# Performance work log

Hardware: AMD Instinct MI355X
Metric: run time of the kernel (lower is better)

The kernel has to match this reference:

```python
import jax, jax.numpy as jnp
import numpy as np

N = 100000  # number of nodes (batch of Irreps objects)
MUL = {'0e': 128, '1o': 64, '2e': 32}  # multiplicities per irrep id
DIM = {'0e': 1, '1o': 3, '2e': 5}      # 2l+1 per irrep id


def setup_inputs() -> dict:
    key = jax.random.key(0)
    ks = jax.random.split(key, 7)
    x0e = jax.random.normal(ks[0], (N, MUL['0e'], DIM['0e']), dtype=jnp.float32)
    x1o = jax.random.normal(ks[1], (N, MUL['1o'], DIM['1o']), dtype=jnp.float32)
    x2e = jax.random.normal(ks[2], (N, MUL['2e'], DIM['2e']), dtype=jnp.float32)
    # one (2l+1)-vector of weights per (output copy, input copy), grouped per irrep id
    w0e = jax.random.normal(ks[3], (MUL['0e'], MUL['0e'], DIM['0e']), dtype=jnp.float32)
    w1o = jax.random.normal(ks[4], (MUL['1o'], MUL['1o'], DIM['1o']), dtype=jnp.float32)
    w2e = jax.random.normal(ks[5], (MUL['2e'], MUL['2e'], DIM['2e']), dtype=jnp.float32)
    bias = jax.random.normal(ks[6], (MUL['0e'],), dtype=jnp.float32)  # one bias per 0e output
    return {"x0e": x0e, "x1o": x1o, "x2e": x2e, "w0e": w0e, "w1o": w1o, "w2e": w2e, "bias": bias}


def reference(x0e, x1o, x2e, w0e, w1o, w2e, bias):
    # Per irrep id: out[n, o, m] = sum_i x[n, i, m] * w[o, i, m]  (elementwise over m)
    y0e = jnp.einsum('nim,oim->nom', x0e, w0e) + bias[None, :, None]
    y1o = jnp.einsum('nim,oim->nom', x1o, w1o)
    y2e = jnp.einsum('nim,oim->nom', x2e, w2e)
    n = x0e.shape[0]
    # Flatten irreps back into a single feature vector per node (sorted id order: 0e, 1o, 2e)
    return jnp.concatenate([y0e.reshape(n, -1), y1o.reshape(n, -1), y2e.reshape(n, -1)], axis=-1)
```

## Files before the change

kernel.cpp:

```cpp
#include <hip/hip_runtime.h>


#define OUT_STRIDE 480

__global__ __launch_bounds__(256) void lin0e_kernel(
    const float* __restrict__ x, const float* __restrict__ w,
    const float* __restrict__ bias, float* __restrict__ out, int n_nodes) {
  __shared__ float wT[128 * 129];
  for (int f = threadIdx.x; f < 128 * 128; f += 256) {
    int o = f >> 7, k = f & 127;
    wT[k * 129 + o] = w[f];
  }
  __syncthreads();

  const int o = threadIdx.x & 127;
  const int half = threadIdx.x >> 7;
  const int n0 = (blockIdx.x * 2 + half) * 16;
  if (n0 >= n_nodes) return;
  const float bv = bias[o];
  const float* __restrict__ xb = x + (size_t)n0 * 128;
  float* __restrict__ ob = out + (size_t)n0 * OUT_STRIDE + o;

  if (n0 + 16 <= n_nodes) {
    float acc[16];
#pragma unroll
    for (int t = 0; t < 16; ++t) acc[t] = 0.f;
#pragma unroll 4
    for (int k = 0; k < 128; ++k) {
      float wv = wT[k * 129 + o];
#pragma unroll
      for (int t = 0; t < 16; ++t)
        acc[t] = fmaf(xb[t * 128 + k], wv, acc[t]);
    }
#pragma unroll
    for (int t = 0; t < 16; ++t) ob[(size_t)t * OUT_STRIDE] = acc[t] + bv;
  } else {
    for (int t = 0; t < n_nodes - n0; ++t) {
      float acc = 0.f;
      for (int k = 0; k < 128; ++k)
        acc = fmaf(xb[t * 128 + k], wT[k * 129 + o], acc);
      ob[(size_t)t * OUT_STRIDE] = acc + bv;
    }
  }
}

__global__ __launch_bounds__(256) void lin1o_kernel(
    const float* __restrict__ x, const float* __restrict__ w,
    float* __restrict__ out, int n_nodes) {
  __shared__ float wT[192 * 65];
  for (int f = threadIdx.x; f < 64 * 192; f += 256) {
    int o = f / 192, j = f - o * 192;
    wT[j * 65 + o] = w[f];
  }
  __syncthreads();

  const int o = threadIdx.x & 63;
  const int wv_ = threadIdx.x >> 6;
  const int n0 = (blockIdx.x * 4 + wv_) * 8;
  if (n0 >= n_nodes) return;
  const float* __restrict__ xb = x + (size_t)n0 * 192;
  float* __restrict__ ob = out + (size_t)n0 * OUT_STRIDE + 128 + o * 3;

  if (n0 + 8 <= n_nodes) {
    float a0[8], a1[8], a2[8];
#pragma unroll
    for (int t = 0; t < 8; ++t) { a0[t] = 0.f; a1[t] = 0.f; a2[t] = 0.f; }
#pragma unroll 2
    for (int k = 0; k < 64; ++k) {
      float w0 = wT[(k * 3 + 0) * 65 + o];
      float w1 = wT[(k * 3 + 1) * 65 + o];
      float w2 = wT[(k * 3 + 2) * 65 + o];
#pragma unroll
      for (int t = 0; t < 8; ++t) {
        a0[t] = fmaf(xb[t * 192 + k * 3 + 0], w0, a0[t]);
        a1[t] = fmaf(xb[t * 192 + k * 3 + 1], w1, a1[t]);
        a2[t] = fmaf(xb[t * 192 + k * 3 + 2], w2, a2[t]);
      }
    }
#pragma unroll
    for (int t = 0; t < 8; ++t) {
      ob[(size_t)t * OUT_STRIDE + 0] = a0[t];
      ob[(size_t)t * OUT_STRIDE + 1] = a1[t];
      ob[(size_t)t * OUT_STRIDE + 2] = a2[t];
    }
  } else {
    for (int t = 0; t < n_nodes - n0; ++t) {
      float a0 = 0.f, a1 = 0.f, a2 = 0.f;
      for (int k = 0; k < 64; ++k) {
        a0 = fmaf(xb[t * 192 + k * 3 + 0], wT[(k * 3 + 0) * 65 + o], a0);
        a1 = fmaf(xb[t * 192 + k * 3 + 1], wT[(k * 3 + 1) * 65 + o], a1);
        a2 = fmaf(xb[t * 192 + k * 3 + 2], wT[(k * 3 + 2) * 65 + o], a2);
      }
      ob[(size_t)t * OUT_STRIDE + 0] = a0;
      ob[(size_t)t * OUT_STRIDE + 1] = a1;
      ob[(size_t)t * OUT_STRIDE + 2] = a2;
    }
  }
}

__global__ __launch_bounds__(256) void lin2e_kernel(
    const float* __restrict__ x, const float* __restrict__ w,
    float* __restrict__ out, int n_nodes) {
  __shared__ float wT[160 * 33];
  for (int f = threadIdx.x; f < 32 * 160; f += 256) {
    int o = f / 160, j = f - o * 160;
    wT[j * 33 + o] = w[f];
  }
  __syncthreads();

  const int o = threadIdx.x & 31;
  const bool store_lane = ((threadIdx.x >> 5) & 1) == 0;
  const int wv_ = threadIdx.x >> 6;
  const int n0 = (blockIdx.x * 4 + wv_) * 8;
  if (n0 >= n_nodes) return;
  const float* __restrict__ xb = x + (size_t)n0 * 160;
  float* __restrict__ ob = out + (size_t)n0 * OUT_STRIDE + 320 + o * 5;

  if (n0 + 8 <= n_nodes) {
    float a[5][8];
#pragma unroll
    for (int m = 0; m < 5; ++m)
#pragma unroll
      for (int t = 0; t < 8; ++t) a[m][t] = 0.f;
    for (int k = 0; k < 32; ++k) {
      float wm[5];
#pragma unroll
      for (int m = 0; m < 5; ++m) wm[m] = wT[(k * 5 + m) * 33 + o];
#pragma unroll
      for (int t = 0; t < 8; ++t) {
#pragma unroll
        for (int m = 0; m < 5; ++m)
          a[m][t] = fmaf(xb[t * 160 + k * 5 + m], wm[m], a[m][t]);
      }
    }
    if (store_lane) {
#pragma unroll
      for (int t = 0; t < 8; ++t) {
#pragma unroll
        for (int m = 0; m < 5; ++m)
          ob[(size_t)t * OUT_STRIDE + m] = a[m][t];
      }
    }
  } else {
    if (store_lane) {
      for (int t = 0; t < n_nodes - n0; ++t) {
        for (int m = 0; m < 5; ++m) {
          float acc = 0.f;
          for (int k = 0; k < 32; ++k)
            acc = fmaf(xb[t * 160 + k * 5 + m], wT[(k * 5 + m) * 33 + o], acc);
          ob[(size_t)t * OUT_STRIDE + m] = acc;
        }
      }
    }
  }
}

extern "C" void kernel_launch(void* const* d_in, const int* in_sizes, int n_in,
                              void* d_out, int out_size, void* d_ws, size_t ws_size,
                              hipStream_t stream) {
  const float* x0e = (const float*)d_in[0];
  const float* x1o = (const float*)d_in[1];
  const float* x2e = (const float*)d_in[2];
  const float* w0e = (const float*)d_in[3];
  const float* w1o = (const float*)d_in[4];
  const float* w2e = (const float*)d_in[5];
  const float* bias = (const float*)d_in[6];
  float* out = (float*)d_out;

  const int n = in_sizes[0] / 128;

  const int b0 = (n + 31) / 32;
  const int b12 = (n + 31) / 32;

  lin0e_kernel<<<b0, 256, 0, stream>>>(x0e, w0e, bias, out, n);
  lin1o_kernel<<<b12, 256, 0, stream>>>(x1o, w1o, out, n);
  lin2e_kernel<<<b12, 256, 0, stream>>>(x2e, w2e, out, n);
}
```

Measured before the change: 859.5 us.

## Unify irrep linears into templated kernel with float4 loads and swizzled weights

Replaces the three per-irrep kernels with one templated kernel. The weights stay in row-major order in shared memory with an XOR swizzle, so each lane reads them as float4. Node features are loaded as float4 with double-buffered register prefetch, and the output channels are split across blocks (HALVES) to cut LDS size and raise occupancy. The aim is fewer scalar global and LDS loads and better latency hiding. The cost is that each block re-reads x for each output half, and register pressure is higher.

```diff
diff --git a/kernel.cpp b/kernel.cpp
--- a/kernel.cpp
+++ b/kernel.cpp
@@ -3,161 +3,121 @@
 
 #define OUT_STRIDE 480
 
-__global__ __launch_bounds__(256) void lin0e_kernel(
+template <int L, int D, int OH, int HALVES, int T, int SEG, bool BIAS, int MINW>
+__global__ __launch_bounds__(256, MINW) void lin_kernel(
     const float* __restrict__ x, const float* __restrict__ w,
     const float* __restrict__ bias, float* __restrict__ out, int n_nodes) {
-  __shared__ float wT[128 * 129];
-  for (int f = threadIdx.x; f < 128 * 128; f += 256) {
-    int o = f >> 7, k = f & 127;
-    wT[k * 129 + o] = w[f];
+  constexpr int NC = L / 4;
+  constexpr int NSTREAM = 256 / OH;
+  __shared__ __align__(16) float wT[OH * L];
+
+  const int ohalf = (HALVES > 1) ? (int)(blockIdx.x & (HALVES - 1)) : 0;
+  const int tile = (HALVES > 1) ? (int)(blockIdx.x >> 1) : (int)blockIdx.x;
+
+  {
+    const float* __restrict__ wseg = w + (size_t)ohalf * OH * L;
+    for (int f = threadIdx.x; f < OH * L; f += 256) {
+      int o = f / L;
+      wT[f ^ ((o & 7) << 2)] = wseg[f];
+    }
   }
   __syncthreads();
 
-  const int o = threadIdx.x & 127;
-  const int half = threadIdx.x >> 7;
-  const int n0 = (blockIdx.x * 2 + half) * 16;
+  const int o = threadIdx.x & (OH - 1);
+  const int stream = threadIdx.x / OH;
+  const int n0 = (tile * NSTREAM + stream) * T;
   if (n0 >= n_nodes) return;
-  const float bv = bias[o];
-  const float* __restrict__ xb = x + (size_t)n0 * 128;
-  float* __restrict__ ob = out + (size_t)n0 * OUT_STRIDE + o;
 
-  if (n0 + 16 <= n_nodes) {
-    float acc[16];
+  const int wrow = o * L;
+  const int swzm = (o & 7) << 2;
+
+  int vzero;
+  asm volatile("v_mov_b32 %0, 0" : "=v"(vzero));
+  const float4* __restrict__ x4 =
+      reinterpret_cast<const float4*>(x + (size_t)n0 * L) + vzero;
+
+  const int og = ohalf * OH + o;
+  float* __restrict__ ob = out + (size_t)n0 * OUT_STRIDE + SEG + og * D;
+  float bv = 0.f;
+  if constexpr (BIAS) bv = bias[og];
+
+#define FMA_CHUNK(JC, XBUF)                                                    \
+  {                                                                            \
+    const float4 wv =                                                          \
+        *reinterpret_cast<const float4*>(&wT[(wrow + 4 * (JC)) ^ swzm]);       \
+    _Pragma("unroll") for (int t = 0; t < T; ++t) {                            \
+      acc[t * D + (4 * (JC) + 0) % D] =                                        \
+          fmaf(XBUF[t].x, wv.x, acc[t * D + (4 * (JC) + 0) % D]);              \
+      acc[t * D + (4 * (JC) + 1) % D] =                                        \
+          fmaf(XBUF[t].y, wv.y, acc[t * D + (4 * (JC) + 1) % D]);              \
+      acc[t * D + (4 * (JC) + 2) % D] =                                        \
+          fmaf(XBUF[t].z, wv.z, acc[t * D + (4 * (JC) + 2) % D]);              \
+      acc[t * D + (4 * (JC) + 3) % D] =                                        \
+          fmaf(XBUF[t].w, wv.w, acc[t * D + (4 * (JC) + 3) % D]);              \
+    }                                                                          \
+  }
+
+  if (n0 + T <= n_nodes) {
+    float acc[T * D];
 #pragma unroll
-    for (int t = 0; t < 16; ++t) acc[t] = 0.f;
-#pragma unroll 4
-    for (int k = 0; k < 128; ++k) {
-      float wv = wT[k * 129 + o];
+    for (int i = 0; i < T * D; ++i) acc[i] = 0.f;
+
+    float4 xa[T], xb[T];
 #pragma unroll
-      for (int t = 0; t < 16; ++t)
-        acc[t] = fmaf(xb[t * 128 + k], wv, acc[t]);
+    for (int t = 0; t < T; ++t) xa[t] = x4[t * NC + 0];
+#pragma unroll
+    for (int t = 0; t < T; ++t) xb[t] = x4[t * NC + 1];
+
+#pragma unroll
+    for (int jc = 0; jc < NC; jc += 2) {
+      FMA_CHUNK(jc, xa);
+      if (jc + 2 < NC) {
+#pragma unroll
+        for (int t = 0; t < T; ++t) xa[t] = x4[t * NC + jc + 2];
+      }
+      FMA_CHUNK(jc + 1, xb);
+      if (jc + 3 < NC) {
+#pragma unroll
+        for (int t = 0; t < T; ++t) xb[t] = x4[t * NC + jc + 3];
+      }
     }
+
 #pragma unroll
-    for (int t = 0; t < 16; ++t) ob[(size_t)t * OUT_STRIDE] = acc[t] + bv;
+    for (int t = 0; t < T; ++t) {
+#pragma unroll
+      for (int m = 0; m < D; ++m)
+        ob[(size_t)t * OUT_STRIDE + m] = acc[t * D + m] + bv;
+    }
   } else {
-    for (int t = 0; t < n_nodes - n0; ++t) {
-      float acc = 0.f;
-      for (int k = 0; k < 128; ++k)
-        acc = fmaf(xb[t * 128 + k], wT[k * 129 + o], acc);
-      ob[(size_t)t * OUT_STRIDE] = acc + bv;
+    const int rem = n_nodes - n0;
+    for (int t = 0; t < rem; ++t) {
+      float accs[D];
+#pragma unroll
+      for (int m = 0; m < D; ++m) accs[m] = 0.f;
+      for (int g = 0; g < NC / D; ++g) {
+#pragma unroll
+        for (int c = 0; c < D; ++c) {
+          const int jc2 = g * D + c;
+          const float4 xv = x4[t * NC + jc2];
+          const float4 wv =
+              *reinterpret_cast<const float4*>(&wT[(wrow + 4 * jc2) ^ swzm]);
+          accs[(4 * c + 0) % D] = fmaf(xv.x, wv.x, accs[(4 * c + 0) % D]);
+          accs[(4 * c + 1) % D] = fmaf(xv.y, wv.y, accs[(4 * c + 1) % D]);
+          accs[(4 * c + 2) % D] = fmaf(xv.z, wv.z, accs[(4 * c + 2) % D]);
+          accs[(4 * c + 3) % D] = fmaf(xv.w, wv.w, accs[(4 * c + 3) % D]);
+        }
+      }
+#pragma unroll
+      for (int m = 0; m < D; ++m)
+        ob[(size_t)t * OUT_STRIDE + m] = accs[m] + bv;
     }
   }
-}
-
-__global__ __launch_bounds__(256) void lin1o_kernel(
-    const float* __restrict__ x, const float* __restrict__ w,
-    float* __restrict__ out, int n_nodes) {
-  __shared__ float wT[192 * 65];
-  for (int f = threadIdx.x; f < 64 * 192; f += 256) {
-    int o = f / 192, j = f - o * 192;
-    wT[j * 65 + o] = w[f];
-  }
-  __syncthreads();
-
-  const int o = threadIdx.x & 63;
-  const int wv_ = threadIdx.x >> 6;
-  const int n0 = (blockIdx.x * 4 + wv_) * 8;
-  if (n0 >= n_nodes) return;
-  const float* __restrict__ xb = x + (size_t)n0 * 192;
-  float* __restrict__ ob = out + (size_t)n0 * OUT_STRIDE + 128 + o * 3;
-
-  if (n0 + 8 <= n_nodes) {
-    float a0[8], a1[8], a2[8];
-#pragma unroll
-    for (int t = 0; t < 8; ++t) { a0[t] = 0.f; a1[t] = 0.f; a2[t] = 0.f; }
-#pragma unroll 2
-    for (int k = 0; k < 64; ++k) {
-      float w0 = wT[(k * 3 + 0) * 65 + o];
-      float w1 = wT[(k * 3 + 1) * 65 + o];
-      float w2 = wT[(k * 3 + 2) * 65 + o];
-#pragma unroll
-      for (int t = 0; t < 8; ++t) {
-        a0[t] = fmaf(xb[t * 192 + k * 3 + 0], w0, a0[t]);
-        a1[t] = fmaf(xb[t * 192 + k * 3 + 1], w1, a1[t]);
-        a2[t] = fmaf(xb[t * 192 + k * 3 + 2], w2, a2[t]);
-      }
-    }
-#pragma unroll
-    for (int t = 0; t < 8; ++t) {
-      ob[(size_t)t * OUT_STRIDE + 0] = a0[t];
-      ob[(size_t)t * OUT_STRIDE + 1] = a1[t];
-      ob[(size_t)t * OUT_STRIDE + 2] = a2[t];
-    }
-  } else {
-    for (int t = 0; t < n_nodes - n0; ++t) {
-      float a0 = 0.f, a1 = 0.f, a2 = 0.f;
-      for (int k = 0; k < 64; ++k) {
-        a0 = fmaf(xb[t * 192 + k * 3 + 0], wT[(k * 3 + 0) * 65 + o], a0);
-        a1 = fmaf(xb[t * 192 + k * 3 + 1], wT[(k * 3 + 1) * 65 + o], a1);
-        a2 = fmaf(xb[t * 192 + k * 3 + 2], wT[(k * 3 + 2) * 65 + o], a2);
-      }
-      ob[(size_t)t * OUT_STRIDE + 0] = a0;
-      ob[(size_t)t * OUT_STRIDE + 1] = a1;
-      ob[(size_t)t * OUT_STRIDE + 2] = a2;
-    }
-  }
-}
-
-__global__ __launch_bounds__(256) void lin2e_kernel(
-    const float* __restrict__ x, const float* __restrict__ w,
-    float* __restrict__ out, int n_nodes) {
-  __shared__ float wT[160 * 33];
-  for (int f = threadIdx.x; f < 32 * 160; f += 256) {
-    int o = f / 160, j = f - o * 160;
-    wT[j * 33 + o] = w[f];
-  }
-  __syncthreads();
-
-  const int o = threadIdx.x & 31;
-  const bool store_lane = ((threadIdx.x >> 5) & 1) == 0;
-  const int wv_ = threadIdx.x >> 6;
-  const int n0 = (blockIdx.x * 4 + wv_) * 8;
-  if (n0 >= n_nodes) return;
-  const float* __restrict__ xb = x + (size_t)n0 * 160;
-  float* __restrict__ ob = out + (size_t)n0 * OUT_STRIDE + 320 + o * 5;
-
-  if (n0 + 8 <= n_nodes) {
-    float a[5][8];
-#pragma unroll
-    for (int m = 0; m < 5; ++m)
-#pragma unroll
-      for (int t = 0; t < 8; ++t) a[m][t] = 0.f;
-    for (int k = 0; k < 32; ++k) {
-      float wm[5];
-#pragma unroll
-      for (int m = 0; m < 5; ++m) wm[m] = wT[(k * 5 + m) * 33 + o];
-#pragma unroll
-      for (int t = 0; t < 8; ++t) {
-#pragma unroll
-        for (int m = 0; m < 5; ++m)
-          a[m][t] = fmaf(xb[t * 160 + k * 5 + m], wm[m], a[m][t]);
-      }
-    }
-    if (store_lane) {
-#pragma unroll
-      for (int t = 0; t < 8; ++t) {
-#pragma unroll
-        for (int m = 0; m < 5; ++m)
-          ob[(size_t)t * OUT_STRIDE + m] = a[m][t];
-      }
-    }
-  } else {
-    if (store_lane) {
-      for (int t = 0; t < n_nodes - n0; ++t) {
-        for (int m = 0; m < 5; ++m) {
-          float acc = 0.f;
-          for (int k = 0; k < 32; ++k)
-            acc = fmaf(xb[t * 160 + k * 5 + m], wT[(k * 5 + m) * 33 + o], acc);
-          ob[(size_t)t * OUT_STRIDE + m] = acc;
-        }
-      }
-    }
-  }
+#undef FMA_CHUNK
 }
 
 extern "C" void kernel_launch(void* const* d_in, const int* in_sizes, int n_in,
-                              void* d_out, int out_size, void* d_ws, size_t ws_size,
-                              hipStream_t stream) {
+                              void* d_out, int out_size, void* d_ws,
+                              size_t ws_size, hipStream_t stream) {
   const float* x0e = (const float*)d_in[0];
   const float* x1o = (const float*)d_in[1];
   const float* x2e = (const float*)d_in[2];
@@ -169,10 +129,15 @@
 
   const int n = in_sizes[0] / 128;
 
-  const int b0 = (n + 31) / 32;
-  const int b12 = (n + 31) / 32;
+  const int tiles0 = (n + 31) / 32;
+  lin_kernel<128, 1, 64, 2, 8, 0, true, 4>
+      <<<tiles0 * 2, 256, 0, stream>>>(x0e, w0e, bias, out, n);
 
-  lin0e_kernel<<<b0, 256, 0, stream>>>(x0e, w0e, bias, out, n);
-  lin1o_kernel<<<b12, 256, 0, stream>>>(x1o, w1o, out, n);
-  lin2e_kernel<<<b12, 256, 0, stream>>>(x2e, w2e, out, n);
+  const int tiles1 = (n + 63) / 64;
+  lin_kernel<192, 3, 32, 2, 8, 128, false, 4>
+      <<<tiles1 * 2, 256, 0, stream>>>(x1o, w1o, nullptr, out, n);
+
+  const int tiles2 = (n + 63) / 64;
+  lin_kernel<160, 5, 32, 1, 8, 320, false, 3>
+      <<<tiles2, 256, 0, stream>>>(x2e, w2e, nullptr, out, n);
 }
```

Measured after the change: 919.3 us. 1.07x slower.
